# Performance work log

Hardware: AMD Instinct MI355X
Metric: run time of the kernel (lower is better)

The kernel has to match this reference:

```python
import jax, jax.numpy as jnp
import numpy as np

EPS = 1e-10
MARGIN = 0.05
DELTA = 0.1
H = W = 512
N = 8388608


def setup_inputs() -> dict:
    key = jax.random.key(0)
    k1, k2, k3, k4 = jax.random.split(key, 4)
    v_input = jax.random.uniform(k1, (3, H, W), dtype=jnp.float32)
    coords = jax.random.randint(k2, (N, 4), 0, W, dtype=jnp.int32)  # x1,y1,x2,y2
    darker = jax.random.randint(k3, (N,), 0, 3, dtype=jnp.int32)
    weights = jax.random.uniform(k4, (N,), dtype=jnp.float32)
    return {"v_input": v_input, "coords": coords, "darker": darker, "weights": weights}


def reference(v_input, coords, darker, weights):
    # v = sum over channels / 3, then affine remap (exactly as torch code)
    v = jnp.sum(v_input, axis=0) / 3.0
    v = (v * 255.0 + 1.0) / 256.0  # [H, W]

    x1, y1, x2, y2 = coords[:, 0], coords[:, 1], coords[:, 2], coords[:, 3]
    r1 = v[y1, x1]
    r2 = v[y2, x2]
    ratio = r1 / (r2 + EPS)
    ratio_inv = r2 / (r1 + EPS)

    b = 1.0 + DELTA + MARGIN
    inv_b = 1.0 / b
    # darker == 1: penalize if ratio > 1/b
    l1 = jnp.where(ratio > inv_b, (ratio - inv_b) + (b - ratio_inv), 0.0)
    # darker == 2: penalize if ratio < b
    l2 = jnp.where(ratio < b, (b - ratio) + (ratio_inv - inv_b), 0.0)
    # darker == 0 (margin <= delta branch): two-sided hinge around [bl, br]
    br = 1.0 + DELTA - MARGIN
    bl = 1.0 / br
    l0 = jnp.where(
        ratio > br,
        (ratio - br) + (bl - ratio_inv),
        jnp.where(ratio < bl, (bl - ratio) + (ratio_inv - br), 0.0),
    )

    per = jnp.where(darker == 1, l1, jnp.where(darker == 2, l2, l0))
    loss = jnp.sum(weights * per) / np.float32(coords.shape[0])
    return loss
```

## Files before the change

kernel.cpp:

```cpp
#include <hip/hip_runtime.h>

#define HW 512
#define NPIX (HW * HW)
#define K 8

#define EPS_F  1e-10f
constexpr double B_d  = 1.0 + 0.1 + 0.05;
constexpr double BR_d = 1.0 + 0.1 - 0.05;
#define B_F    ((float)B_d)
#define INVB_F ((float)(1.0 / B_d))
#define BR_F   ((float)BR_d)
#define BL_F   ((float)(1.0 / BR_d))

typedef __attribute__((ext_vector_type(4))) int ivec4;

__global__ void build_v(const float* __restrict__ vin, _Float16* __restrict__ v,
                        float* __restrict__ out) {
    int i = blockIdx.x * blockDim.x + threadIdx.x;
    if (i == 0) *out = 0.0f;
    if (i < NPIX) {
        float s = vin[i] + vin[i + NPIX] + vin[i + 2 * NPIX];
        float m = s * (1.0f / 3.0f);
        v[i] = (_Float16)((m * 255.0f + 1.0f) * (1.0f / 256.0f));
    }
}

__device__ __forceinline__ float per_loss(float r1, float r2, int d) {
    float ratio = r1 / (r2 + EPS_F);
    float rinv  = r2 / (r1 + EPS_F);
    float l1 = (ratio > INVB_F) ? (ratio - INVB_F + (B_F - rinv)) : 0.0f;
    float l2 = (ratio < B_F)    ? (B_F - ratio + (rinv - INVB_F)) : 0.0f;
    float l0 = (ratio > BR_F)   ? (ratio - BR_F + (BL_F - rinv))
             : ((ratio < BL_F)  ? (BL_F - ratio + (rinv - BR_F)) : 0.0f);
    return (d == 1) ? l1 : ((d == 2) ? l2 : l0);
}

__global__ __launch_bounds__(256) void whdr_kernel(
        const _Float16* __restrict__ v,
        const ivec4* __restrict__ coords,
        const int*   __restrict__ darker,
        const float* __restrict__ weights,
        float*       __restrict__ out,
        int n) {
    const int tid = blockIdx.x * blockDim.x + threadIdx.x;
    const int T   = gridDim.x * blockDim.x;
    float acc = 0.0f;

    if (tid + (K - 1) * T < n) {
        ivec4 c[K];
        #pragma unroll
        for (int k = 0; k < K; ++k) c[k] = __builtin_nontemporal_load(&coords[tid + k * T]);
        float r1[K], r2[K];
        #pragma unroll
        for (int k = 0; k < K; ++k) {
            r1[k] = (float)v[c[k].y * HW + c[k].x];
            r2[k] = (float)v[c[k].w * HW + c[k].z];
        }
        int   dk[K];
        float w[K];
        #pragma unroll
        for (int k = 0; k < K; ++k) dk[k] = __builtin_nontemporal_load(&darker[tid + k * T]);
        #pragma unroll
        for (int k = 0; k < K; ++k) w[k]  = __builtin_nontemporal_load(&weights[tid + k * T]);
        __builtin_amdgcn_sched_barrier(0);
        #pragma unroll
        for (int k = 0; k < K; ++k) acc += w[k] * per_loss(r1[k], r2[k], dk[k]);
    } else {
        for (int i = tid; i < n; i += T) {
            ivec4 c = coords[i];
            float a = (float)v[c.y * HW + c.x];
            float b = (float)v[c.w * HW + c.z];
            acc += weights[i] * per_loss(a, b, darker[i]);
        }
    }

    #pragma unroll
    for (int off = 32; off > 0; off >>= 1)
        acc += __shfl_down(acc, off, 64);
    __shared__ float wsum[4];
    int lane = threadIdx.x & 63;
    int wid  = threadIdx.x >> 6;
    if (lane == 0) wsum[wid] = acc;
    __syncthreads();
    if (threadIdx.x == 0) {
        float s = wsum[0] + wsum[1] + wsum[2] + wsum[3];
        atomicAdd(out, s * (1.0f / 8388608.0f));
    }
}

extern "C" void kernel_launch(void* const* d_in, const int* in_sizes, int n_in,
                              void* d_out, int out_size, void* d_ws, size_t ws_size,
                              hipStream_t stream) {
    const float* v_input = (const float*)d_in[0];
    const ivec4* coords  = (const ivec4*)d_in[1];
    const int*   darker  = (const int*)d_in[2];
    const float* weights = (const float*)d_in[3];
    float* out = (float*)d_out;
    _Float16* v = (_Float16*)d_ws;
    int n = in_sizes[2];

    build_v<<<(NPIX + 255) / 256, 256, 0, stream>>>(v_input, v, out);
    whdr_kernel<<<4096, 256, 0, stream>>>(v, coords, darker, weights, out, n);
}
```

Measured before the change: 276.9 us.

## Quantize brightness map to uint8 and stage a quarter of it in LDS

Stores the averaged brightness map as 8-bit integers instead of fp16, and rebuilds the value as (q+1)/256 at use time. Each 512-thread block copies the first 64K pixels into shared memory, so those lookups skip global gathers. The launch moves to 2048 blocks of 512 threads. This aims to cut gather traffic to global memory, but every block adds a 64KB LDS fill that limits occupancy. The 8-bit rounding also adds error against the continuous reference values.

```diff
diff --git a/kernel.cpp b/kernel.cpp
--- a/kernel.cpp
+++ b/kernel.cpp
@@ -2,7 +2,10 @@
 
 #define HW 512
 #define NPIX (HW * HW)
+#define LDS_PIX 65536
 #define K 8
+#define THREADS 512
+#define BLOCKS 2048
 
 #define EPS_F  1e-10f
 constexpr double B_d  = 1.0 + 0.1 + 0.05;
@@ -14,14 +17,15 @@
 
 typedef __attribute__((ext_vector_type(4))) int ivec4;
 
-__global__ void build_v(const float* __restrict__ vin, _Float16* __restrict__ v,
+__global__ void build_v(const float* __restrict__ vin,
+                        unsigned char* __restrict__ vq,
                         float* __restrict__ out) {
     int i = blockIdx.x * blockDim.x + threadIdx.x;
     if (i == 0) *out = 0.0f;
     if (i < NPIX) {
         float s = vin[i] + vin[i + NPIX] + vin[i + 2 * NPIX];
         float m = s * (1.0f / 3.0f);
-        v[i] = (_Float16)((m * 255.0f + 1.0f) * (1.0f / 256.0f));
+        vq[i] = (unsigned char)__float2int_rn(m * 255.0f);
     }
 }
 
@@ -35,26 +39,38 @@
     return (d == 1) ? l1 : ((d == 2) ? l2 : l0);
 }
 
-__global__ __launch_bounds__(256) void whdr_kernel(
-        const _Float16* __restrict__ v,
+__global__ __launch_bounds__(THREADS) void whdr_kernel(
+        const unsigned char* __restrict__ vq,
         const ivec4* __restrict__ coords,
         const int*   __restrict__ darker,
         const float* __restrict__ weights,
         float*       __restrict__ out,
         int n) {
-    const int tid = blockIdx.x * blockDim.x + threadIdx.x;
-    const int T   = gridDim.x * blockDim.x;
+    __shared__ unsigned char lv[LDS_PIX];
+    {
+        const uint4* s4 = (const uint4*)vq;
+        uint4* d4 = (uint4*)lv;
+        #pragma unroll
+        for (int j = threadIdx.x; j < LDS_PIX / 16; j += THREADS) d4[j] = s4[j];
+    }
+    __syncthreads();
+
+    const int tid = blockIdx.x * THREADS + threadIdx.x;
+    const int T   = gridDim.x * THREADS;
     float acc = 0.0f;
 
     if (tid + (K - 1) * T < n) {
         ivec4 c[K];
         #pragma unroll
         for (int k = 0; k < K; ++k) c[k] = __builtin_nontemporal_load(&coords[tid + k * T]);
-        float r1[K], r2[K];
+        int i1[K], i2[K];
+        #pragma unroll
+        for (int k = 0; k < K; ++k) { i1[k] = c[k].y * HW + c[k].x; i2[k] = c[k].w * HW + c[k].z; }
+        unsigned q1[K], q2[K];
         #pragma unroll
         for (int k = 0; k < K; ++k) {
-            r1[k] = (float)v[c[k].y * HW + c[k].x];
-            r2[k] = (float)v[c[k].w * HW + c[k].z];
+            if (i1[k] < LDS_PIX) q1[k] = lv[i1[k]]; else q1[k] = vq[i1[k]];
+            if (i2[k] < LDS_PIX) q2[k] = lv[i2[k]]; else q2[k] = vq[i2[k]];
         }
         int   dk[K];
         float w[K];
@@ -64,12 +80,16 @@
         for (int k = 0; k < K; ++k) w[k]  = __builtin_nontemporal_load(&weights[tid + k * T]);
         __builtin_amdgcn_sched_barrier(0);
         #pragma unroll
-        for (int k = 0; k < K; ++k) acc += w[k] * per_loss(r1[k], r2[k], dk[k]);
+        for (int k = 0; k < K; ++k) {
+            float r1 = (float)(q1[k] + 1) * (1.0f / 256.0f);
+            float r2 = (float)(q2[k] + 1) * (1.0f / 256.0f);
+            acc += w[k] * per_loss(r1, r2, dk[k]);
+        }
     } else {
         for (int i = tid; i < n; i += T) {
             ivec4 c = coords[i];
-            float a = (float)v[c.y * HW + c.x];
-            float b = (float)v[c.w * HW + c.z];
+            float a = (float)(vq[c.y * HW + c.x] + 1) * (1.0f / 256.0f);
+            float b = (float)(vq[c.w * HW + c.z] + 1) * (1.0f / 256.0f);
             acc += weights[i] * per_loss(a, b, darker[i]);
         }
     }
@@ -77,13 +97,16 @@
     #pragma unroll
     for (int off = 32; off > 0; off >>= 1)
         acc += __shfl_down(acc, off, 64);
-    __shared__ float wsum[4];
+    __syncthreads();
+    float* wsum = (float*)lv;
     int lane = threadIdx.x & 63;
     int wid  = threadIdx.x >> 6;
     if (lane == 0) wsum[wid] = acc;
     __syncthreads();
     if (threadIdx.x == 0) {
-        float s = wsum[0] + wsum[1] + wsum[2] + wsum[3];
+        float s = 0.0f;
+        #pragma unroll
+        for (int i = 0; i < THREADS / 64; ++i) s += wsum[i];
         atomicAdd(out, s * (1.0f / 8388608.0f));
     }
 }
@@ -96,9 +119,9 @@
     const int*   darker  = (const int*)d_in[2];
     const float* weights = (const float*)d_in[3];
     float* out = (float*)d_out;
-    _Float16* v = (_Float16*)d_ws;
+    unsigned char* vq = (unsigned char*)d_ws;
     int n = in_sizes[2];
 
-    build_v<<<(NPIX + 255) / 256, 256, 0, stream>>>(v_input, v, out);
-    whdr_kernel<<<4096, 256, 0, stream>>>(v, coords, darker, weights, out, n);
+    build_v<<<(NPIX + 255) / 256, 256, 0, stream>>>(v_input, vq, out);
+    whdr_kernel<<<BLOCKS, THREADS, 0, stream>>>(vq, coords, darker, weights, out, n);
 }
```

Result: faster. 269.1 us (-2.8%).
